# Kernel optimization log

Hardware: AMD Instinct MI355X
Metric: run time of the kernel (lower is better)

Reference implementation:

```python
import jax, jax.numpy as jnp
import numpy as np

HIDDEN = 768
HEADS = 12
HEAD_DIM = HIDDEN // HEADS
ORDER = 5


def setup_inputs() -> dict:
    key = jax.random.key(0)
    ks = jax.random.split(key, 8)
    s = 0.02
    return {
        "hidden_states": jax.random.normal(ks[0], (4, 2048, HIDDEN), jnp.float32),
        "Wq": jax.random.normal(ks[1], (HIDDEN, HIDDEN), jnp.float32) * s,
        "bq": jnp.zeros((HIDDEN,), jnp.float32),
        "Wk": jax.random.normal(ks[2], (HIDDEN, HIDDEN), jnp.float32) * s,
        "bk": jnp.zeros((HIDDEN,), jnp.float32),
        "Wv": jax.random.normal(ks[3], (HIDDEN, HIDDEN), jnp.float32) * s,
        "bv": jnp.zeros((HIDDEN,), jnp.float32),
        "alphas": jax.random.normal(ks[4], (HEADS, ORDER + 1), jnp.float32) * s,
    }


def _chebyshev_bias(alphas, seq_len, dtype):
    pos = jnp.arange(seq_len, dtype=dtype)
    # rel[i, j] = j - i, normalized to [-1, 1]
    denom = dtype.type(max(seq_len - 1, 1)) if hasattr(dtype, 'type') else float(max(seq_len - 1, 1))
    x = jnp.clip((pos[None, :] - pos[:, None]) / float(max(seq_len - 1, 1)), -1.0, 1.0)
    t0 = jnp.ones_like(x)
    polys = [t0, x]
    for _ in range(2, ORDER + 1):
        polys.append(2.0 * x * polys[-1] - polys[-2])
    tk = jnp.stack(polys, axis=-1)  # [S, S, order+1]
    return jnp.einsum('hk,ijk->hij', alphas, tk)  # [H, S, S]


def reference(hidden_states, Wq, bq, Wk, bk, Wv, bv, alphas):
    b, s, _ = hidden_states.shape

    def split_heads(t):
        return t.reshape(b, s, HEADS, HEAD_DIM).transpose(0, 2, 1, 3)

    q = split_heads(hidden_states @ Wq.T + bq)  # [B, H, S, D]
    k = split_heads(hidden_states @ Wk.T + bk)
    v = split_heads(hidden_states @ Wv.T + bv)

    scores = jnp.einsum('bhid,bhjd->bhij', q, k) / jnp.sqrt(
        jnp.asarray(HEAD_DIM, hidden_states.dtype))
    scores = scores + _chebyshev_bias(alphas, s, hidden_states.dtype)[None]
    probs = jax.nn.softmax(scores, axis=-1)
    ctx = jnp.einsum('bhij,bhjd->bhid', probs, v)  # [B, H, S, D]
    return ctx.transpose(0, 2, 1, 3).reshape(b, s, HIDDEN)
```

## Files before the change

kernel.cpp:

```cpp
#include <hip/hip_runtime.h>
#include <hip/hip_fp16.h>

#define HIDDEN 768
#define HEADS 12
#define HDIM 64
#define SEQ 2048
#define BATCH 4
#define ORDER 5
#define LOG2E 1.44269504088896f

typedef _Float16 f16;
typedef _Float16 f16x8 __attribute__((ext_vector_type(8)));
typedef _Float16 f16x4 __attribute__((ext_vector_type(4)));
typedef float f32x4 __attribute__((ext_vector_type(4)));

#define MFMA16x16x32(A, B, C) __builtin_amdgcn_mfma_f32_16x16x32_f16(A, B, C, 0, 0, 0)

#define GLD16(gptr, lptr)                                                     \
    __builtin_amdgcn_global_load_lds(                                         \
        (const __attribute__((address_space(1))) void*)(gptr),                \
        (__attribute__((address_space(3))) void*)(lptr), 16, 0, 0)

#define NXG (8192 * 768 / 8)
#define NWG (768 * 768 / 8)
#define NCVT (NXG + 3 * NWG)
#define NBIAS (HEADS * (2 * SEQ - 1))

__global__ __launch_bounds__(256)
void prep_kernel(const float* __restrict__ X,
                 const float* __restrict__ Wq, const float* __restrict__ Wk,
                 const float* __restrict__ Wv, const float* __restrict__ alphas,
                 f16* __restrict__ Xh, f16* __restrict__ Wh,
                 float* __restrict__ biasTab)
{
    const int tid = blockIdx.x * 256 + threadIdx.x;
    if (tid < NCVT) {
        const float* src;
        f16* dst;
        size_t off;
        if (tid < NXG)               { src = X;  dst = Xh;              off = (size_t)tid * 8; }
        else if (tid < NXG + NWG)    { src = Wq; dst = Wh;              off = (size_t)(tid - NXG) * 8; }
        else if (tid < NXG + 2*NWG)  { src = Wk; dst = Wh + 768 * 768;  off = (size_t)(tid - NXG - NWG) * 8; }
        else                         { src = Wv; dst = Wh + 2*768*768;  off = (size_t)(tid - NXG - 2*NWG) * 8; }
        float4 a = *(const float4*)(src + off);
        float4 b = *(const float4*)(src + off + 4);
        f16x8 h;
        h[0] = (f16)a.x; h[1] = (f16)a.y; h[2] = (f16)a.z; h[3] = (f16)a.w;
        h[4] = (f16)b.x; h[5] = (f16)b.y; h[6] = (f16)b.z; h[7] = (f16)b.w;
        *(f16x8*)(dst + off) = h;
    } else {
        int idx = tid - NCVT;
        if (idx >= NBIAS) return;
        const int W = 2 * SEQ - 1;
        int h = idx / W;
        int t = idx - h * W;
        float x = (float)(t - (SEQ - 1)) / (float)(SEQ - 1);
        float tp = 1.0f;
        float tc = x;
        float acc = alphas[h * (ORDER + 1) + 0] * tp + alphas[h * (ORDER + 1) + 1] * tc;
#pragma unroll
        for (int k = 2; k <= ORDER; ++k) {
            float tn = 2.0f * x * tc - tp;
            acc += alphas[h * (ORDER + 1) + k] * tn;
            tp = tc; tc = tn;
        }
        biasTab[idx] = acc * LOG2E;
    }
}

__global__ __launch_bounds__(256)
void qkv_kernel(const f16* __restrict__ Xh, const f16* __restrict__ Wh,
                const float* __restrict__ bq, const float* __restrict__ bk,
                const float* __restrict__ bv,
                f16* __restrict__ qf, f16* __restrict__ kf, f16* __restrict__ vtf)
{
    const int wgid = (blockIdx.x & 7) * 144 + (blockIdx.x >> 3);
    const int tileM = wgid / 18;
    const int tileN = wgid % 18;
    const int m0 = tileM * 128;
    const int n0g = tileN * 128;
    const int w = tileN / 6;
    const int nloc0 = n0g - w * 768;
    const float* __restrict__ bias = (w == 0) ? bq : (w == 1) ? bk : bv;

    __shared__ __align__(16) f16 sA[128][32];
    __shared__ __align__(16) f16 sB[128][32];

    const int t = threadIdx.x;
    const int lane = t & 63;
    const int wv = t >> 6;
    const int wm = wv >> 1, wn = wv & 1;
    const int fr = lane & 15;
    const int kg = lane >> 4;

    const int srow = lane >> 2;
    const int scol = (lane & 3) * 8;

    f32x4 acc[4][4];
#pragma unroll
    for (int i = 0; i < 4; ++i)
#pragma unroll
        for (int j = 0; j < 4; ++j) acc[i][j] = (f32x4)(0.0f);

    const f16* gA = Xh + (size_t)(m0 + wv * 32 + srow) * 768 + scol;
    const f16* gB = Wh + (size_t)(n0g + wv * 32 + srow) * 768 + scol;
    f16* lA0 = &sA[wv * 32][0];
    f16* lA1 = &sA[wv * 32 + 16][0];
    f16* lB0 = &sB[wv * 32][0];
    f16* lB1 = &sB[wv * 32 + 16][0];

    for (int kt = 0; kt < 768; kt += 32) {
        __syncthreads();
        GLD16(gA + kt, lA0);
        GLD16(gA + kt + 16 * 768, lA1);
        GLD16(gB + kt, lB0);
        GLD16(gB + kt + 16 * 768, lB1);
        __syncthreads();

        f16x8 af[4], bf[4];
#pragma unroll
        for (int i = 0; i < 4; ++i) {
            af[i] = *(const f16x8*)&sA[wm * 64 + i * 16 + fr][kg * 8];
            bf[i] = *(const f16x8*)&sB[wn * 64 + i * 16 + fr][kg * 8];
        }
#pragma unroll
        for (int mi = 0; mi < 4; ++mi)
#pragma unroll
            for (int ni = 0; ni < 4; ++ni)
                acc[mi][ni] = MFMA16x16x32(af[mi], bf[ni], acc[mi][ni]);
    }

    const int bb = m0 >> 11;
#pragma unroll
    for (int mi = 0; mi < 4; ++mi) {
        const int s0 = (m0 & 2047) + wm * 64 + mi * 16 + kg * 4;
#pragma unroll
        for (int ni = 0; ni < 4; ++ni) {
            const int nloc = nloc0 + wn * 64 + ni * 16 + fr;
            const int hh = nloc >> 6, d = nloc & 63;
            const size_t bh = (size_t)bb * HEADS + hh;
            const float bc = bias[nloc];
            if (w == 2) {
                f16x4 pv;
#pragma unroll
                for (int r = 0; r < 4; ++r) pv[r] = (f16)(acc[mi][ni][r] + bc);
                *(f16x4*)&vtf[(bh * HDIM + d) * SEQ + s0] = pv;
            } else if (w == 0) {
#pragma unroll
                for (int r = 0; r < 4; ++r)
                    qf[(bh * SEQ + s0 + r) * HDIM + d] =
                        (f16)((acc[mi][ni][r] + bc) * (0.125f * LOG2E));
            } else {
#pragma unroll
                for (int r = 0; r < 4; ++r)
                    kf[(bh * SEQ + s0 + r) * HDIM + d] = (f16)(acc[mi][ni][r] + bc);
            }
        }
    }
}

struct __align__(16) SMem {
    union {
        struct {
            f16 sK[64][64];
            f16 sVT[64][64];
        } kv;
        float sO[4][16][72];
    } u;
    f16 sP[4][32][64];
    float sBias[2176];
};

__global__ __launch_bounds__(256, 3)
void attn_kernel(const f16* __restrict__ qf, const f16* __restrict__ kf,
                 const f16* __restrict__ vtf, const float* __restrict__ biasTab,
                 float* __restrict__ out)
{
    const int xcd = blockIdx.x & 7;
    const int ii = blockIdx.x >> 3;
    const int qt = ii & 15;
    const int bh = (ii >> 4) * 8 + xcd;
    const int h = bh % HEADS;
    const int b = bh / HEADS;
    const int q0 = qt * 128;

    __shared__ SMem sm;

    const int t = threadIdx.x;
    const int lane = t & 63;
    const int wv = t >> 6;
    const int fr = lane & 15;
    const int kg = lane >> 4;
    const int r7 = fr & 7;

    {
        const float* bsrc = biasTab + (size_t)h * (2 * SEQ - 1) + 1920 - q0;
        for (int u = t; u < 2175; u += 256) sm.sBias[u] = bsrc[u];
    }

    f16x8 aq[2][2];
#pragma unroll
    for (int s = 0; s < 2; ++s)
#pragma unroll
        for (int c = 0; c < 2; ++c)
            aq[s][c] = *(const f16x8*)(qf +
                ((size_t)bh * SEQ + q0 + wv * 32 + s * 16 + fr) * HDIM + c * 32 + kg * 8);

    f32x4 oacc[2][4];
    float lsum[2] = {0.0f, 0.0f};
#pragma unroll
    for (int s = 0; s < 2; ++s)
#pragma unroll
        for (int df = 0; df < 4; ++df) oacc[s][df] = (f32x4)(0.0f);

    const int srow = t >> 2;
    const int scol = (t & 3) * 16;
    const int sw0 = 8 * (((t & 3) * 2) ^ (srow & 7));
    const int sw1 = 8 * (((t & 3) * 2 + 1) ^ (srow & 7));
    const f16* const gkb = kf + ((size_t)bh * SEQ + srow) * HDIM + scol;
    const f16* const gvb = vtf + ((size_t)bh * HDIM + srow) * SEQ + scol;
    f16* const myP = &sm.sP[wv][0][0];

    f16x8 rk0, rk1, rv0, rv1;
    auto stage_load = [&](int j0) {
        rk0 = *(const f16x8*)(gkb + (size_t)j0 * HDIM);
        rk1 = *(const f16x8*)(gkb + (size_t)j0 * HDIM + 8);
        rv0 = *(const f16x8*)(gvb + j0);
        rv1 = *(const f16x8*)(gvb + j0 + 8);
    };
    auto stage_write = [&]() {
        *(f16x8*)&sm.u.kv.sK[srow][sw0]  = rk0;
        *(f16x8*)&sm.u.kv.sK[srow][sw1]  = rk1;
        *(f16x8*)&sm.u.kv.sVT[srow][sw0] = rv0;
        *(f16x8*)&sm.u.kv.sVT[srow][sw1] = rv1;
    };

    stage_load(0);
    stage_write();
    __syncthreads();

    for (int j0 = 0; j0 < SEQ; j0 += 64) {
        const bool more = (j0 + 64 < SEQ);
        if (more) stage_load(j0 + 64);

        const int ub = j0 + kg * 4 - wv * 32 - fr + 127;
        float bbv[5][4];
#pragma unroll
        for (int g = 0; g < 5; ++g)
#pragma unroll
            for (int r = 0; r < 4; ++r)
                bbv[g][r] = sm.sBias[ub + (g - 1) * 16 + r];

        f32x4 tt[2][4];
#pragma unroll
        for (int s = 0; s < 2; ++s)
#pragma unroll
            for (int ni = 0; ni < 4; ++ni)
#pragma unroll
                for (int r = 0; r < 4; ++r) tt[s][ni][r] = bbv[ni - s + 1][r];

        __builtin_amdgcn_s_setprio(1);
#pragma unroll
        for (int ni = 0; ni < 4; ++ni) {
            const f16* kb = &sm.u.kv.sK[ni * 16 + fr][0];
            f16x8 bk0 = *(const f16x8*)(kb + 8 * (kg ^ r7));
            f16x8 bk1 = *(const f16x8*)(kb + 8 * ((kg + 4) ^ r7));
            tt[0][ni] = MFMA16x16x32(bk0, aq[0][0], tt[0][ni]);
            tt[0][ni] = MFMA16x16x32(bk1, aq[0][1], tt[0][ni]);
            tt[1][ni] = MFMA16x16x32(bk0, aq[1][0], tt[1][ni]);
            tt[1][ni] = MFMA16x16x32(bk1, aq[1][1], tt[1][ni]);
        }
        __builtin_amdgcn_s_setprio(0);

#pragma unroll
        for (int s = 0; s < 2; ++s) {
            float ls = 0.0f;
#pragma unroll
            for (int ni = 0; ni < 4; ++ni) {
                f16x4 ph;
#pragma unroll
                for (int r = 0; r < 4; ++r) {
                    float p = __builtin_amdgcn_exp2f(tt[s][ni][r]);
                    ls += p;
                    ph[r] = (f16)p;
                }
                *(f16x4*)(myP + (s * 16 + fr) * 64 +
                          (((ni * 2 + (kg >> 1)) ^ r7) * 8) + (kg & 1) * 4) = ph;
            }
            lsum[s] += ls;
        }

        f16x8 ap00 = *(const f16x8*)(myP + fr * 64 + 8 * (kg ^ r7));
        f16x8 ap01 = *(const f16x8*)(myP + fr * 64 + 8 * ((kg + 4) ^ r7));
        f16x8 ap10 = *(const f16x8*)(myP + (16 + fr) * 64 + 8 * (kg ^ r7));
        f16x8 ap11 = *(const f16x8*)(myP + (16 + fr) * 64 + 8 * ((kg + 4) ^ r7));
        __builtin_amdgcn_s_setprio(1);
#pragma unroll
        for (int df = 0; df < 4; ++df) {
            const f16* vb = &sm.u.kv.sVT[df * 16 + fr][0];
            f16x8 bv0 = *(const f16x8*)(vb + 8 * (kg ^ r7));
            f16x8 bv1 = *(const f16x8*)(vb + 8 * ((kg + 4) ^ r7));
            oacc[0][df] = MFMA16x16x32(bv0, ap00, oacc[0][df]);
            oacc[0][df] = MFMA16x16x32(bv1, ap01, oacc[0][df]);
            oacc[1][df] = MFMA16x16x32(bv0, ap10, oacc[1][df]);
            oacc[1][df] = MFMA16x16x32(bv1, ap11, oacc[1][df]);
        }
        __builtin_amdgcn_s_setprio(0);

        __syncthreads();
        if (more) {
            stage_write();
            __syncthreads();
        }
    }

    float inv[2];
#pragma unroll
    for (int s = 0; s < 2; ++s) {
        float l = lsum[s];
        l += __shfl_xor(l, 16, 64);
        l += __shfl_xor(l, 32, 64);
        inv[s] = 1.0f / l;
    }

    __syncthreads();
#pragma unroll
    for (int s = 0; s < 2; ++s) {
#pragma unroll
        for (int df = 0; df < 4; ++df) {
            f32x4 v = oacc[s][df];
            v *= inv[s];
            *(f32x4*)&sm.u.sO[wv][fr][df * 16 + kg * 4] = v;
        }
        int row = lane >> 2;
        int cb = (lane & 3) * 16;
        float* dst = out + ((size_t)b * SEQ + q0 + wv * 32 + s * 16 + row) * HIDDEN
                         + h * HDIM + cb;
#pragma unroll
        for (int i = 0; i < 4; ++i) {
            f32x4 v = *(const f32x4*)&sm.u.sO[wv][row][cb + 4 * i];
            *(f32x4*)(dst + 4 * i) = v;
        }
    }
}

extern "C" void kernel_launch(void* const* d_in, const int* in_sizes, int n_in,
                              void* d_out, int out_size, void* d_ws, size_t ws_size,
                              hipStream_t stream) {
    const float* X      = (const float*)d_in[0];
    const float* Wq     = (const float*)d_in[1];
    const float* bq     = (const float*)d_in[2];
    const float* Wk     = (const float*)d_in[3];
    const float* bk     = (const float*)d_in[4];
    const float* Wv     = (const float*)d_in[5];
    const float* bv     = (const float*)d_in[6];
    const float* alphas = (const float*)d_in[7];
    float* out = (float*)d_out;

    const size_t nQ = (size_t)BATCH * HEADS * SEQ * HDIM;
    f16* qf  = (f16*)d_ws;
    f16* kf  = qf + nQ;
    f16* vtf = kf + nQ;
    float* biasTab = (float*)(vtf + nQ);
    f16* Xh = (f16*)(biasTab + 49152);
    f16* Wh = Xh + (size_t)8192 * 768;

    const int prep_threads = NCVT + NBIAS;
    hipLaunchKernelGGL(prep_kernel, dim3((prep_threads + 255) / 256), dim3(256), 0,
                       stream, X, Wq, Wk, Wv, alphas, Xh, Wh, biasTab);
    hipLaunchKernelGGL(qkv_kernel, dim3(1152), dim3(256), 0, stream,
                       Xh, Wh, bq, bk, bv, qf, kf, vtf);
    hipLaunchKernelGGL(attn_kernel, dim3(BATCH * HEADS * 16), dim3(256), 0, stream,
                       qf, kf, vtf, biasTab, out);
}
```

Baseline: 133.6 us.

## Split attention block into 8 waves of 16 query rows each

The attention kernel now runs 512 threads per block, with 8 waves each owning 16 query rows instead of 4 waves owning 32. Per-wave registers for Q fragments, score tiles and output accumulators are halved. K/V tile staging is spread across more threads, and the output writeback is done in two phases that reuse the shared scratch. The aim is more parallelism to hide latency, traded against each wave doing less MFMA work per shared K/V fragment load and a higher launch-bounds occupancy target.

```diff
diff --git a/kernel.cpp b/kernel.cpp
--- a/kernel.cpp
+++ b/kernel.cpp
@@ -165,13 +165,13 @@
             f16 sK[64][64];
             f16 sVT[64][64];
         } kv;
-        float sO[4][16][72];
+        float sO[4][16][68];
     } u;
-    f16 sP[4][32][64];
+    f16 sP[8][16][64];
     float sBias[2176];
 };
 
-__global__ __launch_bounds__(256, 3)
+__global__ __launch_bounds__(512, 6)
 void attn_kernel(const f16* __restrict__ qf, const f16* __restrict__ kf,
                  const f16* __restrict__ vtf, const float* __restrict__ biasTab,
                  float* __restrict__ out)
@@ -195,44 +195,35 @@
 
     {
         const float* bsrc = biasTab + (size_t)h * (2 * SEQ - 1) + 1920 - q0;
-        for (int u = t; u < 2175; u += 256) sm.sBias[u] = bsrc[u];
-    }
-
-    f16x8 aq[2][2];
-#pragma unroll
-    for (int s = 0; s < 2; ++s)
-#pragma unroll
-        for (int c = 0; c < 2; ++c)
-            aq[s][c] = *(const f16x8*)(qf +
-                ((size_t)bh * SEQ + q0 + wv * 32 + s * 16 + fr) * HDIM + c * 32 + kg * 8);
-
-    f32x4 oacc[2][4];
-    float lsum[2] = {0.0f, 0.0f};
-#pragma unroll
-    for (int s = 0; s < 2; ++s)
-#pragma unroll
-        for (int df = 0; df < 4; ++df) oacc[s][df] = (f32x4)(0.0f);
-
-    const int srow = t >> 2;
-    const int scol = (t & 3) * 16;
-    const int sw0 = 8 * (((t & 3) * 2) ^ (srow & 7));
-    const int sw1 = 8 * (((t & 3) * 2 + 1) ^ (srow & 7));
-    const f16* const gkb = kf + ((size_t)bh * SEQ + srow) * HDIM + scol;
-    const f16* const gvb = vtf + ((size_t)bh * HDIM + srow) * SEQ + scol;
+        for (int u = t; u < 2175; u += 512) sm.sBias[u] = bsrc[u];
+    }
+
+    f16x8 aq0 = *(const f16x8*)(qf +
+        ((size_t)bh * SEQ + q0 + wv * 16 + fr) * HDIM + kg * 8);
+    f16x8 aq1 = *(const f16x8*)(qf +
+        ((size_t)bh * SEQ + q0 + wv * 16 + fr) * HDIM + 32 + kg * 8);
+
+    f32x4 oacc[4];
+    float lsum = 0.0f;
+#pragma unroll
+    for (int df = 0; df < 4; ++df) oacc[df] = (f32x4)(0.0f);
+
+    const int srow = t >> 3;
+    const int c8 = t & 7;
+    const int swz = 8 * (c8 ^ (srow & 7));
+    const f16* const gkb = kf + ((size_t)bh * SEQ + srow) * HDIM + c8 * 8;
+    const f16* const gvb = vtf + ((size_t)bh * HDIM + srow) * SEQ + c8 * 8;
     f16* const myP = &sm.sP[wv][0][0];
-
-    f16x8 rk0, rk1, rv0, rv1;
+    const int ubl = kg * 4 - wv * 16 - fr + 127;
+
+    f16x8 rk, rv;
     auto stage_load = [&](int j0) {
-        rk0 = *(const f16x8*)(gkb + (size_t)j0 * HDIM);
-        rk1 = *(const f16x8*)(gkb + (size_t)j0 * HDIM + 8);
-        rv0 = *(const f16x8*)(gvb + j0);
-        rv1 = *(const f16x8*)(gvb + j0 + 8);
+        rk = *(const f16x8*)(gkb + (size_t)j0 * HDIM);
+        rv = *(const f16x8*)(gvb + j0);
     };
     auto stage_write = [&]() {
-        *(f16x8*)&sm.u.kv.sK[srow][sw0]  = rk0;
-        *(f16x8*)&sm.u.kv.sK[srow][sw1]  = rk1;
-        *(f16x8*)&sm.u.kv.sVT[srow][sw0] = rv0;
-        *(f16x8*)&sm.u.kv.sVT[srow][sw1] = rv1;
+        *(f16x8*)&sm.u.kv.sK[srow][swz]  = rk;
+        *(f16x8*)&sm.u.kv.sVT[srow][swz] = rv;
     };
 
     stage_load(0);
@@ -243,21 +234,19 @@
         const bool more = (j0 + 64 < SEQ);
         if (more) stage_load(j0 + 64);
 
-        const int ub = j0 + kg * 4 - wv * 32 - fr + 127;
-        float bbv[5][4];
-#pragma unroll
-        for (int g = 0; g < 5; ++g)
+        const int ub = j0 + ubl;
+        float bbv[4][4];
+#pragma unroll
+        for (int ni = 0; ni < 4; ++ni)
 #pragma unroll
             for (int r = 0; r < 4; ++r)
-                bbv[g][r] = sm.sBias[ub + (g - 1) * 16 + r];
-
-        f32x4 tt[2][4];
-#pragma unroll
-        for (int s = 0; s < 2; ++s)
-#pragma unroll
-            for (int ni = 0; ni < 4; ++ni)
-#pragma unroll
-                for (int r = 0; r < 4; ++r) tt[s][ni][r] = bbv[ni - s + 1][r];
+                bbv[ni][r] = sm.sBias[ub + ni * 16 + r];
+
+        f32x4 tt[4];
+#pragma unroll
+        for (int ni = 0; ni < 4; ++ni)
+#pragma unroll
+            for (int r = 0; r < 4; ++r) tt[ni][r] = bbv[ni][r];
 
         __builtin_amdgcn_s_setprio(1);
 #pragma unroll
@@ -265,45 +254,38 @@
             const f16* kb = &sm.u.kv.sK[ni * 16 + fr][0];
             f16x8 bk0 = *(const f16x8*)(kb + 8 * (kg ^ r7));
             f16x8 bk1 = *(const f16x8*)(kb + 8 * ((kg + 4) ^ r7));
-            tt[0][ni] = MFMA16x16x32(bk0, aq[0][0], tt[0][ni]);
-            tt[0][ni] = MFMA16x16x32(bk1, aq[0][1], tt[0][ni]);
-            tt[1][ni] = MFMA16x16x32(bk0, aq[1][0], tt[1][ni]);
-            tt[1][ni] = MFMA16x16x32(bk1, aq[1][1], tt[1][ni]);
+            tt[ni] = MFMA16x16x32(bk0, aq0, tt[ni]);
+            tt[ni] = MFMA16x16x32(bk1, aq1, tt[ni]);
         }
         __builtin_amdgcn_s_setprio(0);
 
-#pragma unroll
-        for (int s = 0; s < 2; ++s) {
+        {
             float ls = 0.0f;
 #pragma unroll
             for (int ni = 0; ni < 4; ++ni) {
                 f16x4 ph;
 #pragma unroll
                 for (int r = 0; r < 4; ++r) {
-                    float p = __builtin_amdgcn_exp2f(tt[s][ni][r]);
+                    float p = __builtin_amdgcn_exp2f(tt[ni][r]);
                     ls += p;
                     ph[r] = (f16)p;
                 }
-                *(f16x4*)(myP + (s * 16 + fr) * 64 +
+                *(f16x4*)(myP + fr * 64 +
                           (((ni * 2 + (kg >> 1)) ^ r7) * 8) + (kg & 1) * 4) = ph;
             }
-            lsum[s] += ls;
-        }
-
-        f16x8 ap00 = *(const f16x8*)(myP + fr * 64 + 8 * (kg ^ r7));
-        f16x8 ap01 = *(const f16x8*)(myP + fr * 64 + 8 * ((kg + 4) ^ r7));
-        f16x8 ap10 = *(const f16x8*)(myP + (16 + fr) * 64 + 8 * (kg ^ r7));
-        f16x8 ap11 = *(const f16x8*)(myP + (16 + fr) * 64 + 8 * ((kg + 4) ^ r7));
+            lsum += ls;
+        }
+
+        f16x8 ap0 = *(const f16x8*)(myP + fr * 64 + 8 * (kg ^ r7));
+        f16x8 ap1 = *(const f16x8*)(myP + fr * 64 + 8 * ((kg + 4) ^ r7));
         __builtin_amdgcn_s_setprio(1);
 #pragma unroll
         for (int df = 0; df < 4; ++df) {
             const f16* vb = &sm.u.kv.sVT[df * 16 + fr][0];
             f16x8 bv0 = *(const f16x8*)(vb + 8 * (kg ^ r7));
             f16x8 bv1 = *(const f16x8*)(vb + 8 * ((kg + 4) ^ r7));
-            oacc[0][df] = MFMA16x16x32(bv0, ap00, oacc[0][df]);
-            oacc[0][df] = MFMA16x16x32(bv1, ap01, oacc[0][df]);
-            oacc[1][df] = MFMA16x16x32(bv0, ap10, oacc[1][df]);
-            oacc[1][df] = MFMA16x16x32(bv1, ap11, oacc[1][df]);
+            oacc[df] = MFMA16x16x32(bv0, ap0, oacc[df]);
+            oacc[df] = MFMA16x16x32(bv1, ap1, oacc[df]);
         }
         __builtin_amdgcn_s_setprio(0);
 
@@ -314,33 +296,33 @@
         }
     }
 
-    float inv[2];
-#pragma unroll
-    for (int s = 0; s < 2; ++s) {
-        float l = lsum[s];
-        l += __shfl_xor(l, 16, 64);
-        l += __shfl_xor(l, 32, 64);
-        inv[s] = 1.0f / l;
-    }
+    float l = lsum;
+    l += __shfl_xor(l, 16, 64);
+    l += __shfl_xor(l, 32, 64);
+    const float inv = 1.0f / l;
 
     __syncthreads();
 #pragma unroll
-    for (int s = 0; s < 2; ++s) {
-#pragma unroll
-        for (int df = 0; df < 4; ++df) {
-            f32x4 v = oacc[s][df];
-            v *= inv[s];
-            *(f32x4*)&sm.u.sO[wv][fr][df * 16 + kg * 4] = v;
-        }
-        int row = lane >> 2;
-        int cb = (lane & 3) * 16;
-        float* dst = out + ((size_t)b * SEQ + q0 + wv * 32 + s * 16 + row) * HIDDEN
-                         + h * HDIM + cb;
-#pragma unroll
-        for (int i = 0; i < 4; ++i) {
-            f32x4 v = *(const f32x4*)&sm.u.sO[wv][row][cb + 4 * i];
-            *(f32x4*)(dst + 4 * i) = v;
-        }
+    for (int ph = 0; ph < 2; ++ph) {
+        if ((wv >> 2) == ph) {
+            float* const so = &sm.u.sO[wv & 3][0][0];
+#pragma unroll
+            for (int df = 0; df < 4; ++df) {
+                f32x4 v = oacc[df];
+                v *= inv;
+                *(f32x4*)(so + fr * 68 + df * 16 + kg * 4) = v;
+            }
+            int row = lane >> 2;
+            int cb = (lane & 3) * 16;
+            float* dst = out + ((size_t)b * SEQ + q0 + wv * 16 + row) * HIDDEN
+                             + h * HDIM + cb;
+#pragma unroll
+            for (int i = 0; i < 4; ++i) {
+                f32x4 v = *(const f32x4*)(so + row * 68 + cb + 4 * i);
+                *(f32x4*)(dst + 4 * i) = v;
+            }
+        }
+        __syncthreads();
     }
 }
 
@@ -370,6 +352,6 @@
                        stream, X, Wq, Wk, Wv, alphas, Xh, Wh, biasTab);
     hipLaunchKernelGGL(qkv_kernel, dim3(1152), dim3(256), 0, stream,
                        Xh, Wh, bq, bk, bv, qf, kf, vtf);
-    hipLaunchKernelGGL(attn_kernel, dim3(BATCH * HEADS * 16), dim3(256), 0, stream,
+    hipLaunchKernelGGL(attn_kernel, dim3(BATCH * HEADS * 16), dim3(512), 0, stream,
                        qf, kf, vtf, biasTab, out);
 }
```

After: 143.2 us. +7.2%, slower.
